# Kernel tuning notes

Hardware: AMD Instinct MI355X
Metric: run time of the kernel (lower is better)

The kernel has to match this reference:

```python
import jax, jax.numpy as jnp
import numpy as np

LN_EPS = 1e-5
BN_EPS = 1e-5
N_TARGETS = 7


def setup_inputs() -> dict:
    key = jax.random.key(0)
    ks = jax.random.split(key, 12)
    B, N, W, Fin = 64, 40, 256, 64
    H, D = 4, 32
    C = H * D  # gat_out = 128
    L, K = 4, 3  # tcn layers / kernel
    FC = 128
    x = jax.random.normal(ks[0], (B, N, W, Fin), dtype=jnp.float32)
    adj = (jax.random.uniform(ks[1], (N, N)) < 0.3).astype(jnp.float32)
    adj = jnp.maximum(adj, jnp.eye(N, dtype=jnp.float32))  # self-loops
    s = 0.05
    return {
        "x": x,
        "adj": adj,
        "gat_w": jax.random.normal(ks[2], (C, Fin), dtype=jnp.float32) * s,
        "a_src": jax.random.normal(ks[3], (H, D), dtype=jnp.float32) * s,
        "a_dst": jax.random.normal(ks[4], (H, D), dtype=jnp.float32) * s,
        "ln_g": jnp.ones((C,), jnp.float32),
        "ln_b": jnp.zeros((C,), jnp.float32),
        "c1w": jax.random.normal(ks[5], (L, C, C, K), dtype=jnp.float32) * s,
        "c1b": jnp.zeros((L, C), jnp.float32),
        "c2w": jax.random.normal(ks[6], (L, C, C, K), dtype=jnp.float32) * s,
        "c2b": jnp.zeros((L, C), jnp.float32),
        "bn1s": jnp.ones((L, C), jnp.float32),
        "bn1b": jnp.zeros((L, C), jnp.float32),
        "bn1m": jnp.zeros((L, C), jnp.float32),
        "bn1v": jnp.ones((L, C), jnp.float32),
        "bn2s": jnp.ones((L, C), jnp.float32),
        "bn2b": jnp.zeros((L, C), jnp.float32),
        "bn2m": jnp.zeros((L, C), jnp.float32),
        "bn2v": jnp.ones((L, C), jnp.float32),
        "f1w": jax.random.normal(ks[7], (FC, C), dtype=jnp.float32) * s,
        "f1b": jnp.zeros((FC,), jnp.float32),
        "f2w": jax.random.normal(ks[8], (1, FC), dtype=jnp.float32) * s,
        "f2b": jnp.zeros((1,), jnp.float32),
    }


def reference(x, adj, gat_w, a_src, a_dst, ln_g, ln_b,
              c1w, c1b, c2w, c2b,
              bn1s, bn1b, bn1m, bn1v, bn2s, bn2b, bn2m, bn2v,
              f1w, f1b, f2w, f2b):
    B, N, W, Fin = x.shape
    H, D = a_src.shape
    C = H * D
    # --- GAT, vectorized over all W timesteps at once (same math as the per-t loop) ---
    h = jnp.einsum('bnwf,of->bnwo', x, gat_w).reshape(B, N, W, H, D)
    e_src = jnp.einsum('bnwhd,hd->bnwh', h, a_src)  # (B,N,W,H)
    e_dst = jnp.einsum('bnwhd,hd->bnwh', h, a_dst)
    # scores[b,i,w,h,j] = leaky_relu(e_src[b,i] + e_dst[b,j])
    scores = e_src[:, :, :, :, None] + jnp.transpose(e_dst, (0, 2, 3, 1))[:, None]  # (B,N,W,H,N)
    scores = jax.nn.leaky_relu(scores, 0.2)
    mask = adj[None, :, None, None, :] != 0
    scores = jnp.where(mask, scores, -1e9)
    attn = jax.nn.softmax(scores, axis=-1)  # softmax over destination j
    gat = jnp.einsum('bnwhj,bjwhd->bnwhd', attn, h).reshape(B, N, W, C)
    # --- LayerNorm over feature dim ---
    mu = gat.mean(-1, keepdims=True)
    var = gat.var(-1, keepdims=True)
    g = (gat - mu) / jnp.sqrt(var + LN_EPS) * ln_g + ln_b
    # --- TCN over per-node temporal sequences: (B*N, C, W) ---
    seq = jnp.transpose(g.reshape(B * N, W, C), (0, 2, 1))
    K = c1w.shape[-1]

    def bn(z, s, b, m, v):
        return (z - m[None, :, None]) / jnp.sqrt(v[None, :, None] + BN_EPS) * s[None, :, None] + b[None, :, None]

    def cconv(z, w, b, dil):
        pad = (K - 1) * dil  # causal left-padding
        y = jax.lax.conv_general_dilated(z, w, window_strides=(1,), padding=[(pad, 0)],
                                         rhs_dilation=(dil,), dimension_numbers=('NCH', 'OIH', 'NCH'))
        return y + b[None, :, None]

    cur = seq
    for i in range(c1w.shape[0]):  # fixed small number of TCN blocks
        dil = 2 ** i
        o = jax.nn.gelu(bn(cconv(cur, c1w[i], c1b[i], dil), bn1s[i], bn1b[i], bn1m[i], bn1v[i]), approximate=False)
        o = jax.nn.gelu(bn(cconv(o, c2w[i], c2b[i], dil), bn2s[i], bn2b[i], bn2m[i], bn2v[i]), approximate=False)
        cur = jax.nn.gelu(o + cur, approximate=False)  # residual is Identity (in_ch == out_ch)
    h_last = cur[:, :, -1].reshape(B, N, C)
    t = h_last[:, :N_TARGETS, :]  # target_indices = range(7)
    z = jax.nn.gelu(jnp.einsum('bnc,hc->bnh', t, f1w) + f1b, approximate=False)
    logits = (jnp.einsum('bnh,oh->bno', z, f2w) + f2b)[..., 0]  # (B, 7)
    return logits
```

## Files before the change

kernel.cpp:

```cpp
#include <hip/hip_runtime.h>
#include <hip/hip_bf16.h>
#include <math.h>

#define Bb   64
#define Nn   40
#define Ww   256
#define FIN  64
#define Hh   4
#define Dd   32
#define Cc   128
#define NT   7
#define FC   128
#define WT   61
#define W0   195
#define PSTRIDE 520
#define HS2  132

#define GTAUS 2
#define NTG   31
#define XPAN  768
#define GROWS 80
#define PREPB 193

#define SEQHI_OFF  0u
#define SEQ_BYTES  (448u * WT * Cc * 2u)
#define SEQLO_OFF  (SEQHI_OFF + SEQ_BYTES)
#define WBH_OFF    (SEQLO_OFF + SEQ_BYTES)
#define WB_BYTES   (8u * 4u * 24u * 64u * 8u * 2u)
#define WBL_OFF    (WBH_OFF + WB_BYTES)
#define PSB_OFF    (WBL_OFF + WB_BYTES)
#define PSS_OFF    (PSB_OFF + 4096u)
#define PSH_OFF    (PSS_OFF + 4096u)
#define WPHASE_US  49152u

typedef __attribute__((ext_vector_type(8)))  short short8;
typedef __attribute__((ext_vector_type(16))) float f32x16;

__device__ __forceinline__ float gelu_exact(float v) {
    const float z = v * 0.70710678118654752440f;
    const float a = fabsf(z);
    const float t = 1.0f / fmaf(0.3275911f, a, 1.0f);
    float p = fmaf(t, 1.061405429f, -1.453152027f);
    p = fmaf(t, p, 1.421413741f);
    p = fmaf(t, p, -0.284496736f);
    p = fmaf(t, p, 0.254829592f);
    p *= t;
    const float e = 1.0f - p * __expf(-a * a);
    const float erfv = copysignf(e, z);
    return 0.5f * v * (1.0f + erfv);
}
__device__ __forceinline__ float b2f(ushort u) {
    union { uint i; float f; } c; c.i = ((uint)u) << 16; return c.f;
}
__device__ __forceinline__ void split_bf16(float v, ushort& h, ushort& l) {
    __hip_bfloat16 bh = __float2bfloat16(v);
    float fh = __bfloat162float(bh);
    __hip_bfloat16 bl = __float2bfloat16(v - fh);
    h = *(ushort*)&bh; l = *(ushort*)&bl;
}

__global__ __launch_bounds__(256) void gat_prep_kernel(
    const float* __restrict__ x, const float* __restrict__ adj,
    const float* __restrict__ gat_w,
    const float* __restrict__ a_src, const float* __restrict__ a_dst,
    const float* __restrict__ ln_g, const float* __restrict__ ln_b,
    const float* __restrict__ c1w, const float* __restrict__ c1b,
    const float* __restrict__ c2w, const float* __restrict__ c2b,
    const float* __restrict__ bn1s, const float* __restrict__ bn1b,
    const float* __restrict__ bn1m, const float* __restrict__ bn1v,
    const float* __restrict__ bn2s, const float* __restrict__ bn2b,
    const float* __restrict__ bn2m, const float* __restrict__ bn2v,
    char* __restrict__ ws,
    ushort* __restrict__ seq_hi, ushort* __restrict__ seq_lo)
{
    __shared__ __align__(16) char pool[2 * 12288];
    __shared__ __align__(16) float h_lds[GROWS * HS2];

    const int tid = threadIdx.x;

    if (blockIdx.x < PREPB) {
        if (blockIdx.x < 192) {
            const int t = blockIdx.x * 256 + tid;
            const int lane  = t & 63;
            const int kstep = (t >> 6) % 24;
            const int nt    = ((t >> 6) / 24) & 3;
            const int p     = (t >> 6) / 96;
            const int l = p >> 1, cv = p & 1;
            const int co = nt * 32 + (lane & 31);
            const float* wsrc = cv ? c2w : c1w;
            ushort* wbh = (ushort*)(ws + WBH_OFF);
            ushort* wbl = (ushort*)(ws + WBL_OFF);
#pragma unroll
            for (int j = 0; j < 8; ++j) {
                const int k  = kstep * 16 + ((lane >> 5) << 3) + j;
                const int kk = k >> 7, ci = k & 127;
                const float w = wsrc[((size_t)(l * Cc + co) * Cc + ci) * 3 + kk];
                ushort h, lo; split_bf16(w, h, lo);
                wbh[(size_t)t * 8 + j] = h;
                wbl[(size_t)t * 8 + j] = lo;
            }
        } else {
            float* psb = (float*)(ws + PSB_OFF);
            float* pss = (float*)(ws + PSS_OFF);
            float* psh = (float*)(ws + PSH_OFF);
            for (int idx = tid; idx < 1024; idx += 256) {
                const int p = idx >> 7, co = idx & 127;
                const int l = p >> 1, cv = p & 1;
                const int lc = l * Cc + co;
                const float s  = cv ? bn2s[lc] : bn1s[lc];
                const float bb = cv ? bn2b[lc] : bn1b[lc];
                const float m  = cv ? bn2m[lc] : bn1m[lc];
                const float vv = cv ? bn2v[lc] : bn1v[lc];
                const float cb = cv ? c2b[lc] : c1b[lc];
                const float scale = s * rsqrtf(vv + 1e-5f);
                pss[idx] = scale;
                psh[idx] = bb - m * scale;
                psb[idx] = cb;
            }
        }
        return;
    }

    ushort* xa_hi = (ushort*)pool;
    ushort* xa_lo = (ushort*)(pool + 12288);
    float* e_lds    = (float*)pool;
    float* attn_lds = (float*)(pool + 2560);
    float* g_lds    = (float*)(pool + 11520);

    const int blk = blockIdx.x - PREPB;
    const int b   = blk / NTG;
    const int tg  = blk % NTG;
    const int tau0g  = tg * GTAUS;
    const int nvalid = (tau0g + 1 < WT) ? 2 : 1;

    for (int idx = tid; idx < GTAUS * Nn * 8; idx += 256) {
        const int tl  = idx >= 320;
        const int rem = idx - tl * 320;
        const int n  = rem >> 3;
        const int oc = rem & 7;
        if (tl < nvalid) {
            const int w = W0 + tau0g + tl;
            const float* src = x + ((size_t)(b * Nn + n) * Ww + w) * FIN + oc * 8;
            const float4 f0 = *(const float4*)(src);
            const float4 f1 = *(const float4*)(src + 4);
            ushort h[8], l[8];
            split_bf16(f0.x, h[0], l[0]); split_bf16(f0.y, h[1], l[1]);
            split_bf16(f0.z, h[2], l[2]); split_bf16(f0.w, h[3], l[3]);
            split_bf16(f1.x, h[4], l[4]); split_bf16(f1.y, h[5], l[5]);
            split_bf16(f1.z, h[6], l[6]); split_bf16(f1.w, h[7], l[7]);
            const int dst = oc * XPAN + (tl * Nn + n) * 8;
            *(uint4*)(xa_hi + dst) = *(uint4*)h;
            *(uint4*)(xa_lo + dst) = *(uint4*)l;
        }
    }
    __syncthreads();

    {
        const int wave = tid >> 6;
        const int lane = tid & 63;
        const int nt   = wave;
        const int q2   = lane >> 5;
        const int m32  = lane & 31;
        const int co   = nt * 32 + m32;

        short8 BH[4], BL[4];
#pragma unroll
        for (int ks = 0; ks < 4; ++ks) {
            const float* gp = gat_w + co * FIN + ks * 16 + q2 * 8;
            const float4 f0 = *(const float4*)(gp);
            const float4 f1 = *(const float4*)(gp + 4);
            ushort h[8], l[8];
            split_bf16(f0.x, h[0], l[0]); split_bf16(f0.y, h[1], l[1]);
            split_bf16(f0.z, h[2], l[2]); split_bf16(f0.w, h[3], l[3]);
            split_bf16(f1.x, h[4], l[4]); split_bf16(f1.y, h[5], l[5]);
            split_bf16(f1.z, h[6], l[6]); split_bf16(f1.w, h[7], l[7]);
            BH[ks] = *(short8*)h;
            BL[ks] = *(short8*)l;
        }

#pragma unroll
        for (int mt = 0; mt < 3; ++mt) {
            f32x16 acc;
#pragma unroll
            for (int i = 0; i < 16; ++i) acc[i] = 0.f;
#pragma unroll
            for (int ks = 0; ks < 4; ++ks) {
                const int aoff = (ks * 2 + q2) * XPAN + (mt * 32 + m32) * 8;
                const short8 ah = *(const short8*)(xa_hi + aoff);
                const short8 al = *(const short8*)(xa_lo + aoff);
                acc = __builtin_amdgcn_mfma_f32_32x32x16_bf16(ah, BH[ks], acc, 0, 0, 0);
                acc = __builtin_amdgcn_mfma_f32_32x32x16_bf16(al, BH[ks], acc, 0, 0, 0);
                acc = __builtin_amdgcn_mfma_f32_32x32x16_bf16(ah, BL[ks], acc, 0, 0, 0);
            }
#pragma unroll
            for (int reg = 0; reg < 16; ++reg) {
                const int row = mt * 32 + (reg & 3) + 8 * (reg >> 2) + 4 * q2;
                if (row < GROWS) h_lds[row * HS2 + co] = acc[reg];
            }
        }
    }
    __syncthreads();

    for (int u = tid; u < GTAUS * 2 * Nn * Hh; u += 256) {
        const int tl = u >= 320;
        const int uu = u - tl * 320;
        const int s  = uu & 1;
        const int hh = (uu >> 1) & 3;
        const int n  = uu >> 3;
        const float* av = (s ? a_dst : a_src) + hh * Dd;
        const float* hp = h_lds + (tl * Nn + n) * HS2 + hh * Dd;
        float acc = 0.f;
#pragma unroll
        for (int i = 0; i < 8; ++i) {
            const float4 hv = *(const float4*)(hp + i * 4);
            const float4 avv = *(const float4*)(av + i * 4);
            acc += hv.x * avv.x + hv.y * avv.y + hv.z * avv.z + hv.w * avv.w;
        }
        e_lds[((tl * 2 + s) * Nn + n) * Hh + hh] = acc;
    }
    __syncthreads();

    if (tid < GTAUS * NT * Hh) {
        const int tl = tid >= NT * Hh;
        const int i  = tid - tl * NT * Hh;
        const int n  = i >> 2;
        const int hh = i & 3;
        if (tl < nvalid) {
            const float es = e_lds[((tl * 2 + 0) * Nn + n) * Hh + hh];
            float sc[Nn];
            float mx = -1e30f;
#pragma unroll
            for (int j = 0; j < Nn; ++j) {
                float s = es + e_lds[((tl * 2 + 1) * Nn + j) * Hh + hh];
                s = (s > 0.f) ? s : 0.2f * s;
                if (adj[n * Nn + j] == 0.0f) s = -1e9f;
                sc[j] = s;
                mx = fmaxf(mx, s);
            }
            float sum = 0.f;
#pragma unroll
            for (int j = 0; j < Nn; ++j) { const float p = expf(sc[j] - mx); sc[j] = p; sum += p; }
            const float inv = 1.0f / sum;
#pragma unroll
            for (int j = 0; j < Nn; ++j)
                attn_lds[((tl * NT + n) * Hh + hh) * Nn + j] = sc[j] * inv;
        }
    }
    __syncthreads();

    for (int u = tid; u < GTAUS * NT * 32; u += 256) {
        const int tl = u >= NT * 32;
        const int i  = u - tl * NT * 32;
        const int n    = i >> 5;
        const int cq   = i & 31;
        const int c0   = cq * 4;
        const int head = cq >> 3;
        if (tl < nvalid) {
            const float* ap = attn_lds + ((tl * NT + n) * Hh + head) * Nn;
            float4 acc = make_float4(0.f, 0.f, 0.f, 0.f);
            for (int j = 0; j < Nn; ++j) {
                const float a = ap[j];
                const float4 hv = *(const float4*)(h_lds + (tl * Nn + j) * HS2 + c0);
                acc.x += a * hv.x; acc.y += a * hv.y;
                acc.z += a * hv.z; acc.w += a * hv.w;
            }
            *(float4*)(g_lds + (tl * NT + n) * Cc + c0) = acc;
        }
    }
    __syncthreads();

    for (int u = tid; u < GTAUS * NT * 32; u += 256) {
        const int tl = u >= NT * 32;
        const int i  = u - tl * NT * 32;
        const int n  = i >> 5;
        const int lane = u & 31;
        if (tl < nvalid) {
            const float4 v = ((const float4*)(g_lds + (tl * NT + n) * Cc))[lane];
            float s  = v.x + v.y + v.z + v.w;
            float sq = v.x*v.x + v.y*v.y + v.z*v.z + v.w*v.w;
#pragma unroll
            for (int off = 16; off; off >>= 1) {
                s  += __shfl_xor(s, off, 32);
                sq += __shfl_xor(sq, off, 32);
            }
            const float mu   = s * (1.0f / Cc);
            const float rstd = rsqrtf(sq * (1.0f / Cc) - mu * mu + 1e-5f);
            const float4 gg = ((const float4*)ln_g)[lane];
            const float4 bb = ((const float4*)ln_b)[lane];
            float o0 = (v.x - mu) * rstd * gg.x + bb.x;
            float o1 = (v.y - mu) * rstd * gg.y + bb.y;
            float o2 = (v.z - mu) * rstd * gg.z + bb.z;
            float o3 = (v.w - mu) * rstd * gg.w + bb.w;
            const int r = b * NT + n;
            const int tau = tau0g + tl;
            ushort4 uh, ul;
            split_bf16(o0, uh.x, ul.x);
            split_bf16(o1, uh.y, ul.y);
            split_bf16(o2, uh.z, ul.z);
            split_bf16(o3, uh.w, ul.w);
            const int p  = (lane >> 2) * 2 + ((lane >> 1) & 1);
            const int j0 = (lane & 1) * 4;
            const size_t off = ((size_t)(r * 16 + p) * WT + tau) * 8 + j0;
            *(ushort4*)(seq_hi + off) = uh;
            *(ushort4*)(seq_lo + off) = ul;
        }
    }
}

__device__ __forceinline__ void conv_sk(
    const ushort* in_hi, const ushort* in_lo,
    ushort* out_hi, ushort* out_lo,
    float* scratch,
    const ushort* __restrict__ wbh, const ushort* __restrict__ wbl,
    const float* __restrict__ psb, const float* __restrict__ pss,
    const float* __restrict__ psh,
    const int tau0, const int d, const int kh, const int nt,
    const int lane, const bool residual)
{
    const int m  = lane & 31;
    const int q2 = lane >> 5;
    const bool skipA = (tau0 > 31);

    int rA0a = m - 2 * d; rA0a = rA0a < 0 ? 0 : rA0a;
    int rA1a = m - d;     rA1a = rA1a < 0 ? 0 : rA1a;
    const int rA2a = m;
    const int rA0b = 32 + m - 2 * d;
    const int rA1b = 32 + m - d;
    const int rA2b = 32 + m;

    const ushort* wb_h = wbh + (size_t)(nt * 24 + kh * 12) * 512 + lane * 8;
    const ushort* wb_l = wbl + (size_t)(nt * 24 + kh * 12) * 512 + lane * 8;

    const int co = nt * 32 + m;
    const float bsv = psb[co], scv = pss[co], shv = psh[co];
    const int colb = ((co >> 4) * 2 + ((co >> 3) & 1)) * PSTRIDE + (co & 7);

    f32x16 accA, accB;
#pragma unroll
    for (int i = 0; i < 16; ++i) { accA[i] = 0.f; accB[i] = 0.f; }

    short8 WH[3], WL[3];
#pragma unroll
    for (int i = 0; i < 3; ++i) {
        WH[i] = *(const short8*)(wb_h + i * 512);
        WL[i] = *(const short8*)(wb_l + i * 512);
    }

#pragma unroll
    for (int i = 0; i < 12; ++i) {
        const int slot = i % 3;
        const short8 bh = WH[slot];
        const short8 bl = WL[slot];
        if (i + 3 < 12) {
            WH[slot] = *(const short8*)(wb_h + (i + 3) * 512);
            WL[slot] = *(const short8*)(wb_l + (i + 3) * 512);
        }
        const int ks = kh * 12 + i;
        const int kk = ks >> 3;
        const int panel = (((ks & 7) << 1) + q2) * PSTRIDE;
        if (!skipA) {
            const int ra = (kk == 0) ? rA0a : (kk == 1 ? rA1a : rA2a);
            const short8 ahA = *(const short8*)(in_hi + panel + ra * 8);
            const short8 alA = *(const short8*)(in_lo + panel + ra * 8);
            accA = __builtin_amdgcn_mfma_f32_32x32x16_bf16(ahA, bh, accA, 0, 0, 0);
            accA = __builtin_amdgcn_mfma_f32_32x32x16_bf16(alA, bh, accA, 0, 0, 0);
            accA = __builtin_amdgcn_mfma_f32_32x32x16_bf16(ahA, bl, accA, 0, 0, 0);
        }
        {
            const int rb = (kk == 0) ? rA0b : (kk == 1 ? rA1b : rA2b);
            const short8 ahB = *(const short8*)(in_hi + panel + rb * 8);
            const short8 alB = *(const short8*)(in_lo + panel + rb * 8);
            accB = __builtin_amdgcn_mfma_f32_32x32x16_bf16(ahB, bh, accB, 0, 0, 0);
            accB = __builtin_amdgcn_mfma_f32_32x32x16_bf16(alB, bh, accB, 0, 0, 0);
            accB = __builtin_amdgcn_mfma_f32_32x32x16_bf16(ahB, bl, accB, 0, 0, 0);
        }
    }

    if (residual) __syncthreads();

    if (kh == 0) {
        float* dst = scratch + ((4 + nt) << 10) + lane;
#pragma unroll
        for (int r = 0; r < 16; ++r) dst[r * 64] = accB[r];
    } else if (!skipA) {
        float* dst = scratch + (nt << 10) + lane;
#pragma unroll
        for (int r = 0; r < 16; ++r) dst[r * 64] = accA[r];
    }
    __syncthreads();

    f32x16 acc;
    if (kh == 0) {
        acc = accA;
        if (!skipA) {
            const float* srcp = scratch + (nt << 10) + lane;
#pragma unroll
            for (int r = 0; r < 16; ++r) acc[r] += srcp[r * 64];
        }
    } else {
        acc = accB;
        const float* srcp = scratch + ((4 + nt) << 10) + lane;
#pragma unroll
        for (int r = 0; r < 16; ++r) acc[r] += srcp[r * 64];
    }

    if (!residual) __syncthreads();

    if (!(skipA && kh == 0)) {
        const int mt = kh;
#pragma unroll
        for (int reg = 0; reg < 16; ++reg) {
            const int row = (reg & 3) + 8 * (reg >> 2) + 4 * q2;
            const int tau = mt * 32 + row;
            if (tau >= tau0 && tau <= 60) {
                float v = (acc[reg] + bsv) * scv + shv;
                v = gelu_exact(v);
                const int off = colb + tau * 8;
                if (residual)
                    v = gelu_exact(v + b2f(out_hi[off]) + b2f(out_lo[off]));
                ushort uh, ul; split_bf16(v, uh, ul);
                out_hi[off] = uh; out_lo[off] = ul;
            }
        }
    }
}

__global__ __launch_bounds__(512, 4) void tcn_head_kernel(
    const char* __restrict__ ws,
    const float* __restrict__ f1w, const float* __restrict__ f1b,
    const float* __restrict__ f2w, const float* __restrict__ f2b,
    float* __restrict__ out)
{
    __shared__ __align__(16) ushort cur_hi[16 * PSTRIDE];
    __shared__ __align__(16) ushort cur_lo[16 * PSTRIDE];
    __shared__ __align__(16) ushort o1_pair[2][16 * PSTRIDE];
    __shared__ float red[FC];

    ushort* o1_hi = o1_pair[0];
    ushort* o1_lo = o1_pair[1];
    float*  scratch = (float*)o1_pair;

    const int tid = threadIdx.x;
    const int r   = blockIdx.x;

    const ushort* seq_hi = (const ushort*)(ws + SEQHI_OFF);
    const ushort* seq_lo = (const ushort*)(ws + SEQLO_OFF);
    const ushort* WBH    = (const ushort*)(ws + WBH_OFF);
    const ushort* WBL    = (const ushort*)(ws + WBL_OFF);
    const float*  PSB    = (const float*)(ws + PSB_OFF);
    const float*  PSS    = (const float*)(ws + PSS_OFF);
    const float*  PSH    = (const float*)(ws + PSH_OFF);

    {
        const size_t base = (size_t)r * (16 * WT * 8);
        for (int i = tid; i < 16 * WT; i += 512) {
            const int p = i / WT, row = i - p * WT;
            const int dst = p * PSTRIDE + row * 8;
            *(uint4*)(cur_hi + dst) = *(const uint4*)(seq_hi + base + i * 8);
            *(uint4*)(cur_lo + dst) = *(const uint4*)(seq_lo + base + i * 8);
        }
    }
    __syncthreads();

    const int wave = tid >> 6;
    const int lane = tid & 63;
    const int nt   = wave & 3;
    const int kh   = wave >> 2;

    const int tau0_1[4] = {2, 8, 20, 44};
    const int tau0_2[4] = {4, 12, 28, 60};

#pragma unroll
    for (int l = 0; l < 4; ++l) {
        const int d  = 1 << l;
        const int p1 = 2 * l, p2 = 2 * l + 1;
        conv_sk(cur_hi, cur_lo, o1_hi, o1_lo, scratch,
                WBH + (size_t)p1 * WPHASE_US, WBL + (size_t)p1 * WPHASE_US,
                PSB + p1 * Cc, PSS + p1 * Cc, PSH + p1 * Cc,
                tau0_1[l], d, kh, nt, lane, false);
        __syncthreads();
        conv_sk(o1_hi, o1_lo, cur_hi, cur_lo, scratch,
                WBH + (size_t)p2 * WPHASE_US, WBL + (size_t)p2 * WPHASE_US,
                PSB + p2 * Cc, PSS + p2 * Cc, PSH + p2 * Cc,
                tau0_2[l], d, kh, nt, lane, true);
        __syncthreads();
    }

    if (tid < FC) {
        const float4* wr = (const float4*)(f1w + tid * Cc);
        float acc = 0.f;
#pragma unroll
        for (int i = 0; i < Cc / 4; ++i) {
            const float4 wv = wr[i];
            const int ci0 = i * 4;
            const int off = ((ci0 >> 4) * 2 + ((ci0 >> 3) & 1)) * PSTRIDE
                          + 60 * 8 + (ci0 & 7);
            const ushort4 vh = *(const ushort4*)(cur_hi + off);
            const ushort4 vl = *(const ushort4*)(cur_lo + off);
            acc += wv.x * (b2f(vh.x) + b2f(vl.x))
                 + wv.y * (b2f(vh.y) + b2f(vl.y))
                 + wv.z * (b2f(vh.z) + b2f(vl.z))
                 + wv.w * (b2f(vh.w) + b2f(vl.w));
        }
        red[tid] = gelu_exact(acc + f1b[tid]) * f2w[tid];
    }
    __syncthreads();
    if (tid < 64) {
        float v = red[tid] + red[tid + 64];
#pragma unroll
        for (int off = 32; off; off >>= 1) v += __shfl_xor(v, off, 64);
        if (tid == 0) out[r] = v + f2b[0];
    }
}

extern "C" void kernel_launch(void* const* d_in, const int* in_sizes, int n_in,
                              void* d_out, int out_size, void* d_ws, size_t ws_size,
                              hipStream_t stream) {
    const float* x     = (const float*)d_in[0];
    const float* adj   = (const float*)d_in[1];
    const float* gat_w = (const float*)d_in[2];
    const float* a_src = (const float*)d_in[3];
    const float* a_dst = (const float*)d_in[4];
    const float* ln_g  = (const float*)d_in[5];
    const float* ln_b  = (const float*)d_in[6];
    const float* c1w   = (const float*)d_in[7];
    const float* c1b   = (const float*)d_in[8];
    const float* c2w   = (const float*)d_in[9];
    const float* c2b   = (const float*)d_in[10];
    const float* bn1s  = (const float*)d_in[11];
    const float* bn1b  = (const float*)d_in[12];
    const float* bn1m  = (const float*)d_in[13];
    const float* bn1v  = (const float*)d_in[14];
    const float* bn2s  = (const float*)d_in[15];
    const float* bn2b  = (const float*)d_in[16];
    const float* bn2m  = (const float*)d_in[17];
    const float* bn2v  = (const float*)d_in[18];
    const float* f1w   = (const float*)d_in[19];
    const float* f1b   = (const float*)d_in[20];
    const float* f2w   = (const float*)d_in[21];
    const float* f2b   = (const float*)d_in[22];

    char* ws = (char*)d_ws;

    gat_prep_kernel<<<PREPB + Bb * NTG, 256, 0, stream>>>(
        x, adj, gat_w, a_src, a_dst, ln_g, ln_b,
        c1w, c1b, c2w, c2b,
        bn1s, bn1b, bn1m, bn1v, bn2s, bn2b, bn2m, bn2v,
        ws, (ushort*)(ws + SEQHI_OFF), (ushort*)(ws + SEQLO_OFF));

    tcn_head_kernel<<<Bb * NT, 512, 0, stream>>>(
        ws, f1w, f1b, f2w, f2b, (float*)d_out);
}
```

Before: 364.6 us.

## Process one timestep per GAT block, deepen weight prefetch, set waves-per-EU hints

The GAT prep kernel now handles one timestep per block instead of two. The grid grows from 64*31 to 64*61 blocks, and LDS per block shrinks, which removes the padding waste of the three-M-tile MFMA over 80 rows (now two tiles over 40 rows). The TCN conv weight prefetch ring goes from 3 to 4 slots. Both kernels get amdgpu_waves_per_eu(4) occupancy hints, replacing the launch_bounds min-blocks argument on the TCN kernel. The trade-off is more blocks, each repeating the gat_w load and split, and higher register pressure from the deeper prefetch.

```diff
diff --git a/kernel.cpp b/kernel.cpp
--- a/kernel.cpp
+++ b/kernel.cpp
@@ -16,10 +16,7 @@
 #define PSTRIDE 520
 #define HS2  132
 
-#define GTAUS 2
-#define NTG   31
-#define XPAN  768
-#define GROWS 80
+#define XPAN1 512
 #define PREPB 193
 
 #define SEQHI_OFF  0u
@@ -59,7 +56,9 @@
     h = *(ushort*)&bh; l = *(ushort*)&bl;
 }
 
-__global__ __launch_bounds__(256) void gat_prep_kernel(
+__global__ __launch_bounds__(256)
+__attribute__((amdgpu_waves_per_eu(4)))
+void gat_prep_kernel(
     const float* __restrict__ x, const float* __restrict__ adj,
     const float* __restrict__ gat_w,
     const float* __restrict__ a_src, const float* __restrict__ a_dst,
@@ -73,8 +72,8 @@
     char* __restrict__ ws,
     ushort* __restrict__ seq_hi, ushort* __restrict__ seq_lo)
 {
-    __shared__ __align__(16) char pool[2 * 12288];
-    __shared__ __align__(16) float h_lds[GROWS * HS2];
+    __shared__ __align__(16) char pool[2 * 8192];
+    __shared__ __align__(16) float h_lds[Nn * HS2];
 
     const int tid = threadIdx.x;
 
@@ -122,36 +121,30 @@
     }
 
     ushort* xa_hi = (ushort*)pool;
-    ushort* xa_lo = (ushort*)(pool + 12288);
+    ushort* xa_lo = (ushort*)(pool + 8192);
     float* e_lds    = (float*)pool;
-    float* attn_lds = (float*)(pool + 2560);
-    float* g_lds    = (float*)(pool + 11520);
+    float* attn_lds = (float*)(pool + 1280);
+    float* g_lds    = (float*)(pool + 5760);
 
     const int blk = blockIdx.x - PREPB;
-    const int b   = blk / NTG;
-    const int tg  = blk % NTG;
-    const int tau0g  = tg * GTAUS;
-    const int nvalid = (tau0g + 1 < WT) ? 2 : 1;
-
-    for (int idx = tid; idx < GTAUS * Nn * 8; idx += 256) {
-        const int tl  = idx >= 320;
-        const int rem = idx - tl * 320;
-        const int n  = rem >> 3;
-        const int oc = rem & 7;
-        if (tl < nvalid) {
-            const int w = W0 + tau0g + tl;
-            const float* src = x + ((size_t)(b * Nn + n) * Ww + w) * FIN + oc * 8;
-            const float4 f0 = *(const float4*)(src);
-            const float4 f1 = *(const float4*)(src + 4);
-            ushort h[8], l[8];
-            split_bf16(f0.x, h[0], l[0]); split_bf16(f0.y, h[1], l[1]);
-            split_bf16(f0.z, h[2], l[2]); split_bf16(f0.w, h[3], l[3]);
-            split_bf16(f1.x, h[4], l[4]); split_bf16(f1.y, h[5], l[5]);
-            split_bf16(f1.z, h[6], l[6]); split_bf16(f1.w, h[7], l[7]);
-            const int dst = oc * XPAN + (tl * Nn + n) * 8;
-            *(uint4*)(xa_hi + dst) = *(uint4*)h;
-            *(uint4*)(xa_lo + dst) = *(uint4*)l;
-        }
+    const int b   = blk / WT;
+    const int tau = blk % WT;
+    const int w   = W0 + tau;
+
+    for (int idx = tid; idx < Nn * 8; idx += 256) {
+        const int n  = idx >> 3;
+        const int oc = idx & 7;
+        const float* src = x + ((size_t)(b * Nn + n) * Ww + w) * FIN + oc * 8;
+        const float4 f0 = *(const float4*)(src);
+        const float4 f1 = *(const float4*)(src + 4);
+        ushort h[8], l[8];
+        split_bf16(f0.x, h[0], l[0]); split_bf16(f0.y, h[1], l[1]);
+        split_bf16(f0.z, h[2], l[2]); split_bf16(f0.w, h[3], l[3]);
+        split_bf16(f1.x, h[4], l[4]); split_bf16(f1.y, h[5], l[5]);
+        split_bf16(f1.z, h[6], l[6]); split_bf16(f1.w, h[7], l[7]);
+        const int dst = oc * XPAN1 + n * 8;
+        *(uint4*)(xa_hi + dst) = *(uint4*)h;
+        *(uint4*)(xa_lo + dst) = *(uint4*)l;
     }
     __syncthreads();
 
@@ -179,13 +172,13 @@
         }
 
 #pragma unroll
-        for (int mt = 0; mt < 3; ++mt) {
+        for (int mt = 0; mt < 2; ++mt) {
             f32x16 acc;
 #pragma unroll
             for (int i = 0; i < 16; ++i) acc[i] = 0.f;
 #pragma unroll
             for (int ks = 0; ks < 4; ++ks) {
-                const int aoff = (ks * 2 + q2) * XPAN + (mt * 32 + m32) * 8;
+                const int aoff = (ks * 2 + q2) * XPAN1 + (mt * 32 + m32) * 8;
                 const short8 ah = *(const short8*)(xa_hi + aoff);
                 const short8 al = *(const short8*)(xa_lo + aoff);
                 acc = __builtin_amdgcn_mfma_f32_32x32x16_bf16(ah, BH[ks], acc, 0, 0, 0);
@@ -195,20 +188,18 @@
 #pragma unroll
             for (int reg = 0; reg < 16; ++reg) {
                 const int row = mt * 32 + (reg & 3) + 8 * (reg >> 2) + 4 * q2;
-                if (row < GROWS) h_lds[row * HS2 + co] = acc[reg];
+                if (row < Nn) h_lds[row * HS2 + co] = acc[reg];
             }
         }
     }
     __syncthreads();
 
-    for (int u = tid; u < GTAUS * 2 * Nn * Hh; u += 256) {
-        const int tl = u >= 320;
-        const int uu = u - tl * 320;
-        const int s  = uu & 1;
-        const int hh = (uu >> 1) & 3;
-        const int n  = uu >> 3;
+    for (int u = tid; u < 2 * Nn * Hh; u += 256) {
+        const int s  = u & 1;
+        const int hh = (u >> 1) & 3;
+        const int n  = u >> 3;
         const float* av = (s ? a_dst : a_src) + hh * Dd;
-        const float* hp = h_lds + (tl * Nn + n) * HS2 + hh * Dd;
+        const float* hp = h_lds + n * HS2 + hh * Dd;
         float acc = 0.f;
 #pragma unroll
         for (int i = 0; i < 8; ++i) {
@@ -216,94 +207,80 @@
             const float4 avv = *(const float4*)(av + i * 4);
             acc += hv.x * avv.x + hv.y * avv.y + hv.z * avv.z + hv.w * avv.w;
         }
-        e_lds[((tl * 2 + s) * Nn + n) * Hh + hh] = acc;
-    }
-    __syncthreads();
-
-    if (tid < GTAUS * NT * Hh) {
-        const int tl = tid >= NT * Hh;
-        const int i  = tid - tl * NT * Hh;
-        const int n  = i >> 2;
-        const int hh = i & 3;
-        if (tl < nvalid) {
-            const float es = e_lds[((tl * 2 + 0) * Nn + n) * Hh + hh];
-            float sc[Nn];
-            float mx = -1e30f;
-#pragma unroll
-            for (int j = 0; j < Nn; ++j) {
-                float s = es + e_lds[((tl * 2 + 1) * Nn + j) * Hh + hh];
-                s = (s > 0.f) ? s : 0.2f * s;
-                if (adj[n * Nn + j] == 0.0f) s = -1e9f;
-                sc[j] = s;
-                mx = fmaxf(mx, s);
-            }
-            float sum = 0.f;
-#pragma unroll
-            for (int j = 0; j < Nn; ++j) { const float p = expf(sc[j] - mx); sc[j] = p; sum += p; }
-            const float inv = 1.0f / sum;
-#pragma unroll
-            for (int j = 0; j < Nn; ++j)
-                attn_lds[((tl * NT + n) * Hh + hh) * Nn + j] = sc[j] * inv;
-        }
-    }
-    __syncthreads();
-
-    for (int u = tid; u < GTAUS * NT * 32; u += 256) {
-        const int tl = u >= NT * 32;
-        const int i  = u - tl * NT * 32;
-        const int n    = i >> 5;
-        const int cq   = i & 31;
+        e_lds[s * (Nn * Hh) + n * Hh + hh] = acc;
+    }
+    __syncthreads();
+
+    if (tid < NT * Hh) {
+        const int n  = tid >> 2;
+        const int hh = tid & 3;
+        const float es = e_lds[n * Hh + hh];
+        float sc[Nn];
+        float mx = -1e30f;
+#pragma unroll
+        for (int j = 0; j < Nn; ++j) {
+            float s = es + e_lds[Nn * Hh + j * Hh + hh];
+            s = (s > 0.f) ? s : 0.2f * s;
+            if (adj[n * Nn + j] == 0.0f) s = -1e9f;
+            sc[j] = s;
+            mx = fmaxf(mx, s);
+        }
+        float sum = 0.f;
+#pragma unroll
+        for (int j = 0; j < Nn; ++j) { const float p = expf(sc[j] - mx); sc[j] = p; sum += p; }
+        const float inv = 1.0f / sum;
+#pragma unroll
+        for (int j = 0; j < Nn; ++j)
+            attn_lds[(n * Hh + hh) * Nn + j] = sc[j] * inv;
+    }
+    __syncthreads();
+
+    if (tid < NT * 32) {
+        const int n    = tid >> 5;
+        const int cq   = tid & 31;
         const int c0   = cq * 4;
         const int head = cq >> 3;
-        if (tl < nvalid) {
-            const float* ap = attn_lds + ((tl * NT + n) * Hh + head) * Nn;
-            float4 acc = make_float4(0.f, 0.f, 0.f, 0.f);
-            for (int j = 0; j < Nn; ++j) {
-                const float a = ap[j];
-                const float4 hv = *(const float4*)(h_lds + (tl * Nn + j) * HS2 + c0);
-                acc.x += a * hv.x; acc.y += a * hv.y;
-                acc.z += a * hv.z; acc.w += a * hv.w;
-            }
-            *(float4*)(g_lds + (tl * NT + n) * Cc + c0) = acc;
-        }
-    }
-    __syncthreads();
-
-    for (int u = tid; u < GTAUS * NT * 32; u += 256) {
-        const int tl = u >= NT * 32;
-        const int i  = u - tl * NT * 32;
-        const int n  = i >> 5;
-        const int lane = u & 31;
-        if (tl < nvalid) {
-            const float4 v = ((const float4*)(g_lds + (tl * NT + n) * Cc))[lane];
-            float s  = v.x + v.y + v.z + v.w;
-            float sq = v.x*v.x + v.y*v.y + v.z*v.z + v.w*v.w;
-#pragma unroll
-            for (int off = 16; off; off >>= 1) {
-                s  += __shfl_xor(s, off, 32);
-                sq += __shfl_xor(sq, off, 32);
-            }
-            const float mu   = s * (1.0f / Cc);
-            const float rstd = rsqrtf(sq * (1.0f / Cc) - mu * mu + 1e-5f);
-            const float4 gg = ((const float4*)ln_g)[lane];
-            const float4 bb = ((const float4*)ln_b)[lane];
-            float o0 = (v.x - mu) * rstd * gg.x + bb.x;
-            float o1 = (v.y - mu) * rstd * gg.y + bb.y;
-            float o2 = (v.z - mu) * rstd * gg.z + bb.z;
-            float o3 = (v.w - mu) * rstd * gg.w + bb.w;
-            const int r = b * NT + n;
-            const int tau = tau0g + tl;
-            ushort4 uh, ul;
-            split_bf16(o0, uh.x, ul.x);
-            split_bf16(o1, uh.y, ul.y);
-            split_bf16(o2, uh.z, ul.z);
-            split_bf16(o3, uh.w, ul.w);
-            const int p  = (lane >> 2) * 2 + ((lane >> 1) & 1);
-            const int j0 = (lane & 1) * 4;
-            const size_t off = ((size_t)(r * 16 + p) * WT + tau) * 8 + j0;
-            *(ushort4*)(seq_hi + off) = uh;
-            *(ushort4*)(seq_lo + off) = ul;
-        }
+        const float* ap = attn_lds + (n * Hh + head) * Nn;
+        float4 acc = make_float4(0.f, 0.f, 0.f, 0.f);
+        for (int j = 0; j < Nn; ++j) {
+            const float a = ap[j];
+            const float4 hv = *(const float4*)(h_lds + j * HS2 + c0);
+            acc.x += a * hv.x; acc.y += a * hv.y;
+            acc.z += a * hv.z; acc.w += a * hv.w;
+        }
+        *(float4*)(g_lds + n * Cc + c0) = acc;
+    }
+    __syncthreads();
+
+    if (tid < NT * 32) {
+        const int n = tid >> 5, lane = tid & 31;
+        const float4 v = ((const float4*)(g_lds + n * Cc))[lane];
+        float s  = v.x + v.y + v.z + v.w;
+        float sq = v.x*v.x + v.y*v.y + v.z*v.z + v.w*v.w;
+#pragma unroll
+        for (int off = 16; off; off >>= 1) {
+            s  += __shfl_xor(s, off, 32);
+            sq += __shfl_xor(sq, off, 32);
+        }
+        const float mu   = s * (1.0f / Cc);
+        const float rstd = rsqrtf(sq * (1.0f / Cc) - mu * mu + 1e-5f);
+        const float4 gg = ((const float4*)ln_g)[lane];
+        const float4 bb = ((const float4*)ln_b)[lane];
+        float o0 = (v.x - mu) * rstd * gg.x + bb.x;
+        float o1 = (v.y - mu) * rstd * gg.y + bb.y;
+        float o2 = (v.z - mu) * rstd * gg.z + bb.z;
+        float o3 = (v.w - mu) * rstd * gg.w + bb.w;
+        const int r = b * NT + n;
+        ushort4 uh, ul;
+        split_bf16(o0, uh.x, ul.x);
+        split_bf16(o1, uh.y, ul.y);
+        split_bf16(o2, uh.z, ul.z);
+        split_bf16(o3, uh.w, ul.w);
+        const int p  = (lane >> 2) * 2 + ((lane >> 1) & 1);
+        const int j0 = (lane & 1) * 4;
+        const size_t off = ((size_t)(r * 16 + p) * WT + tau) * 8 + j0;
+        *(ushort4*)(seq_hi + off) = uh;
+        *(ushort4*)(seq_lo + off) = ul;
     }
 }
 
@@ -339,21 +316,21 @@
 #pragma unroll
     for (int i = 0; i < 16; ++i) { accA[i] = 0.f; accB[i] = 0.f; }
 
-    short8 WH[3], WL[3];
-#pragma unroll
-    for (int i = 0; i < 3; ++i) {
+    short8 WH[4], WL[4];
+#pragma unroll
+    for (int i = 0; i < 4; ++i) {
         WH[i] = *(const short8*)(wb_h + i * 512);
         WL[i] = *(const short8*)(wb_l + i * 512);
     }
 
 #pragma unroll
     for (int i = 0; i < 12; ++i) {
-        const int slot = i % 3;
+        const int slot = i & 3;
         const short8 bh = WH[slot];
         const short8 bl = WL[slot];
-        if (i + 3 < 12) {
-            WH[slot] = *(const short8*)(wb_h + (i + 3) * 512);
-            WL[slot] = *(const short8*)(wb_l + (i + 3) * 512);
+        if (i + 4 < 12) {
+            WH[slot] = *(const short8*)(wb_h + (i + 4) * 512);
+            WL[slot] = *(const short8*)(wb_l + (i + 4) * 512);
         }
         const int ks = kh * 12 + i;
         const int kk = ks >> 3;
@@ -425,7 +402,9 @@
     }
 }
 
-__global__ __launch_bounds__(512, 4) void tcn_head_kernel(
+__global__ __launch_bounds__(512)
+__attribute__((amdgpu_waves_per_eu(4)))
+void tcn_head_kernel(
     const char* __restrict__ ws,
     const float* __restrict__ f1w, const float* __restrict__ f1b,
     const float* __restrict__ f2w, const float* __restrict__ f2b,
@@ -542,7 +521,7 @@
 
     char* ws = (char*)d_ws;
 
-    gat_prep_kernel<<<PREPB + Bb * NTG, 256, 0, stream>>>(
+    gat_prep_kernel<<<PREPB + Bb * WT, 256, 0, stream>>>(
         x, adj, gat_w, a_src, a_dst, ln_g, ln_b,
         c1w, c1b, c2w, c2b,
         bn1s, bn1b, bn1m, bn1v, bn2s, bn2b, bn2m, bn2v,
```

Measured after the change: 367.1 us. Within noise of the previous version (+0.7%).
